# Kernel tuning notes

Hardware: AMD Instinct MI355X
Metric: run time of the kernel (lower is better)

## Reference

```python
import jax, jax.numpy as jnp
import numpy as np

B, D, M = 4, 3, 64
N2, N1, N0 = 512, 2048, 8192   # points per sample: coarse -> fine
C2, C1, C0 = 256, 128, 64
K = 3

def setup_inputs() -> dict:
    key = jax.random.key(0)
    ks = jax.random.split(key, 16)
    def nrm(k, shp, s=1.0):
        return jax.random.normal(k, shp, dtype=jnp.float32) * s
    return {
        "par_embedding": nrm(ks[0], (B, 1, M)),
        "x": nrm(ks[1], (B * N2, C2)),
        "pos": jax.random.uniform(ks[2], (B * N2, D), dtype=jnp.float32),
        "batch": jnp.repeat(jnp.arange(B), N2),
        "x_skip_l1": nrm(ks[3], (B * N1, C1)),
        "pos_skip_l1": jax.random.uniform(ks[4], (B * N1, D), dtype=jnp.float32),
        "batch_skip_l1": jnp.repeat(jnp.arange(B), N1),
        "x_skip_l0": nrm(ks[5], (B * N0, C0)),
        "pos_skip_l0": jax.random.uniform(ks[6], (B * N0, D), dtype=jnp.float32),
        "batch_skip_l0": jnp.repeat(jnp.arange(B), N0),
        # FP layer 0 MLP [C2+C1, 256, 128], plain_last=False; par_reduce -> 128
        "W0a": nrm(ks[7], (C2 + C1, 256), 0.05), "b0a": jnp.zeros((256,), jnp.float32),
        "W0b": nrm(ks[8], (256, 128), 0.05),     "b0b": jnp.zeros((128,), jnp.float32),
        "Wp0": nrm(ks[9], (M, 128), 0.05),       "bp0": jnp.zeros((128,), jnp.float32),
        # FP layer 1 MLP [128+C0, 128, 64], plain_last=True; par_reduce -> 64
        "W1a": nrm(ks[10], (128 + C0, 128), 0.05), "b1a": jnp.zeros((128,), jnp.float32),
        "W1b": nrm(ks[11], (128, 64), 0.05),       "b1b": jnp.zeros((64,), jnp.float32),
        "Wp1": nrm(ks[12], (M, 64), 0.05),         "bp1": jnp.zeros((64,), jnp.float32),
    }

def knn_interpolate(x, pos, pos_tgt, batch_size, k):
    """torch_geometric.nn.knn_interpolate with equal-size per-sample blocks.
    knn indices and inverse-squared-distance weights are non-differentiable
    (computed under no_grad in torch), hence stop_gradient."""
    C = x.shape[-1]
    xs = x.reshape(batch_size, -1, C)          # (B, ns, C)
    ps = pos.reshape(batch_size, -1, D)        # (B, ns, D)
    pt = pos_tgt.reshape(batch_size, -1, D)    # (B, nt, D)
    d2 = jnp.sum((pt[:, :, None, :] - ps[:, None, :, :]) ** 2, axis=-1)  # (B, nt, ns)
    d2 = jax.lax.stop_gradient(d2)
    neg_d2, idx = jax.lax.top_k(-d2, k)                                   # (B, nt, k)
    w = 1.0 / jnp.maximum(-neg_d2, 1e-16)
    feats = jax.vmap(lambda xb, ib: xb[ib])(xs, idx)                      # (B, nt, k, C)
    out = jnp.sum(feats * w[..., None], axis=2) / jnp.sum(w, axis=2, keepdims=True)
    return out.reshape(-1, C)

def fp_layer(par, x, pos, x_skip, pos_skip, k, Wa, ba, Wb, bb, Wp, bp, plain_last):
    bsz = par.shape[0]
    x = knn_interpolate(x, pos, pos_skip, bsz, k)
    x = jnp.concatenate([x, x_skip], axis=1)
    x = jnp.tanh(x @ Wa + ba)
    x = x @ Wb + bb
    if not plain_last:
        x = jnp.tanh(x)
    n = x.shape[0] // bsz
    p = jnp.tanh(par.reshape(bsz, -1) @ Wp + bp)     # (B, Cout)
    return x * jnp.repeat(p, n, axis=0)               # broadcast branch vector per sample

def reference(par_embedding, x, pos, batch, x_skip_l1, pos_skip_l1, batch_skip_l1,
              x_skip_l0, pos_skip_l0, batch_skip_l0,
              W0a, b0a, W0b, b0b, Wp0, bp0, W1a, b1a, W1b, b1b, Wp1, bp1):
    # skips[::-1]: coarser skip (level 1) consumed first, finest (level 0) last
    x1 = fp_layer(par_embedding, x, pos, x_skip_l1, pos_skip_l1, K,
                  W0a, b0a, W0b, b0b, Wp0, bp0, plain_last=False)
    x0 = fp_layer(par_embedding, x1, pos_skip_l1, x_skip_l0, pos_skip_l0, K,
                  W1a, b1a, W1b, b1b, Wp1, bp1, plain_last=True)
    return (x0, pos_skip_l0, batch_skip_l0)
```

## Files before the change

### kernel.cpp

```cpp
#include <hip/hip_runtime.h>
#include <hip/hip_bf16.h>

using bf16 = __hip_bfloat16;
using v8s = __attribute__((ext_vector_type(8))) short;
using v4f = __attribute__((ext_vector_type(4))) float;

constexpr int kB = 4, kM = 64;
constexpr int kN2 = 512, kN1 = 2048, kN0 = 8192;
constexpr int kC2 = 256, kC1 = 128, kC0 = 64;

__device__ __forceinline__ float bs2f(unsigned short u) {
    return __uint_as_float((unsigned)u << 16);
}
__device__ __forceinline__ unsigned short f2bs(float f) {
    unsigned u = __float_as_uint(f);
    u += 0x7FFFu + ((u >> 16) & 1u);
    return (unsigned short)(u >> 16);
}
__device__ __forceinline__ float rdIn(const void* p, long i, int f32) {
    return f32 ? ((const float*)p)[i] : bs2f(((const unsigned short*)p)[i]);
}
__device__ __forceinline__ unsigned short rdBS(const void* p, long i, int f32) {
    return f32 ? f2bs(((const float*)p)[i]) : ((const unsigned short*)p)[i];
}
__device__ __forceinline__ void ld8(const void* p, long off, int f32, float v[8]) {
    if (f32) {
        const float* fp = (const float*)p + off;
        float4 a = *(const float4*)fp;
        float4 b = *(const float4*)(fp + 4);
        v[0] = a.x; v[1] = a.y; v[2] = a.z; v[3] = a.w;
        v[4] = b.x; v[5] = b.y; v[6] = b.z; v[7] = b.w;
    } else {
        const unsigned short* hp = (const unsigned short*)p + off;
        uint4 u = *(const uint4*)hp;
        unsigned w[4] = {u.x, u.y, u.z, u.w};
        #pragma unroll
        for (int i = 0; i < 4; i++) {
            v[2 * i]     = bs2f((unsigned short)(w[i] & 0xFFFFu));
            v[2 * i + 1] = bs2f((unsigned short)(w[i] >> 16));
        }
    }
}
__device__ __forceinline__ uint4 pack8(const unsigned short o[8]) {
    uint4 u;
    u.x = (unsigned)o[0] | ((unsigned)o[1] << 16);
    u.y = (unsigned)o[2] | ((unsigned)o[3] << 16);
    u.z = (unsigned)o[4] | ((unsigned)o[5] << 16);
    u.w = (unsigned)o[6] | ((unsigned)o[7] << 16);
    return u;
}

__global__ void fpno_guard(float code, float* __restrict__ out) {
    if (threadIdx.x == 0) out[0] = code;
}

__global__ __launch_bounds__(512) void fpno_p1(
    const unsigned int* __restrict__ posW,
    const void* __restrict__ pos,
    const void* __restrict__ pos1,
    const void* __restrict__ pos0,
    const void* __restrict__ W0a, const void* __restrict__ W0b,
    const void* __restrict__ W1a, const void* __restrict__ W1b,
    const void* __restrict__ par,
    const void* __restrict__ Wp0, const void* __restrict__ bp0,
    const void* __restrict__ Wp1, const void* __restrict__ bp1,
    const int* __restrict__ bt0,
    int* __restrict__ flag, unsigned short* __restrict__ WT,
    float* __restrict__ g0, float* __restrict__ g1,
    int* __restrict__ i1d, float* __restrict__ w1d,
    float4* __restrict__ ptsG, int* __restrict__ cstG,
    float4* __restrict__ ptsT, int* __restrict__ cstT,
    float* __restrict__ out) {
    #pragma clang fp contract(off)
    __shared__ __align__(16) char smem[20480];
    __shared__ int sflg[2];
    const int b = blockIdx.x, tid = threadIdx.x;

    if (tid == 0) { sflg[0] = 0; sflg[1] = 0; }
    __syncthreads();
    {
        unsigned lo = posW[tid] & 0xFFFFu;
        int bad = 0, nz = 0;
        if (lo != 0u) { nz = 1; if ((lo & 0x8000u) || lo > 0x3F80u) bad = 1; }
        if (bad) sflg[0] = 1;
        if (nz) sflg[1] = 1;
    }
    __syncthreads();
    const int f32 = (sflg[0] || !sflg[1]) ? 1 : 0;
    if (b == 0 && tid == 0) *flag = f32;

    if (b < 320) {
        int id = b * 512 + tid;
        const void* src; int N; int base, local;
        if      (id < 98304)  { src = W0a; N = 256; base = 0;      local = id; }
        else if (id < 131072) { src = W0b; N = 128; base = 98304;  local = id - 98304; }
        else if (id < 155648) { src = W1a; N = 128; base = 131072; local = id - 131072; }
        else                  { src = W1b; N = 64;  base = 155648; local = id - 155648; }
        int NT = N >> 4;
        int e = local & 7;
        int l = (local >> 3) & 63;
        int rest = local >> 9;
        int t = rest % NT;
        int kc = rest / NT;
        int n = t * 16 + (l & 15);
        int k = kc * 32 + ((l >> 4) << 3) + e;
        WT[base + local] = rdBS(src, (long)k * N + n, f32);
    } else if (b < 322) {
        int id = (b - 320) * 512 + tid;
        if (id < kB * 128) {
            int bb = id / 128, n = id % 128;
            float a = rdIn(bp0, n, f32);
            for (int m = 0; m < kM; m++)
                a += rdIn(par, bb * kM + m, f32) * rdIn(Wp0, m * 128 + n, f32);
            g0[id] = tanhf(a);
        } else if (id < kB * 128 + kB * 64) {
            int id2 = id - kB * 128;
            int bb = id2 / 64, n = id2 % 64;
            float a = rdIn(bp1, n, f32);
            for (int m = 0; m < kM; m++)
                a += rdIn(par, bb * kM + m, f32) * rdIn(Wp1, m * 64 + n, f32);
            g1[id2] = tanhf(a);
        }
    } else if (b < 450) {
        constexpr int NS = kN2;
        float4* sp = (float4*)smem;
        float*  cd = (float*)(smem + 8192);
        int*    ci = (int*)(smem + 14336);
        const int blk = b - 322;
        const int tLoc = tid >> 3;
        const int spl  = tid & 7;
        const int tGlob = blk * 64 + tLoc;
        const int smp = tGlob / kN1;
        for (int i = tid; i < NS; i += 512) {
            long bb = (long)(smp * NS + i) * 3;
            sp[i] = make_float4(rdIn(pos, bb, f32), rdIn(pos, bb + 1, f32),
                                rdIn(pos, bb + 2, f32), 0.f);
        }
        __syncthreads();
        long tb = (long)tGlob * 3;
        float px = rdIn(pos1, tb, f32), py = rdIn(pos1, tb + 1, f32),
              pz = rdIn(pos1, tb + 2, f32);
        float d0 = 1e30f, d1 = 1e30f, d2 = 1e30f;
        int i0 = 0x7FFFFFFF, i1 = 0x7FFFFFFF, i2 = 0x7FFFFFFF;
        for (int j = spl; j < NS; j += 8) {
            float4 s = sp[j];
            float dx = px - s.x, dy = py - s.y, dz = pz - s.z;
            float d = ((dx * dx) + (dy * dy)) + (dz * dz);
            bool l0 = d < d0, l1 = d < d1, l2 = d < d2;
            float nd2 = l1 ? d1 : (l2 ? d : d2);
            int   ni2 = l1 ? i1 : (l2 ? j : i2);
            float nd1 = l0 ? d0 : (l1 ? d : d1);
            int   ni1 = l0 ? i0 : (l1 ? j : i1);
            float nd0 = l0 ? d : d0;
            int   ni0 = l0 ? j : i0;
            d2 = nd2; i2 = ni2; d1 = nd1; i1 = ni1; d0 = nd0; i0 = ni0;
        }
        cd[tid * 3 + 0] = d0; ci[tid * 3 + 0] = i0;
        cd[tid * 3 + 1] = d1; ci[tid * 3 + 1] = i1;
        cd[tid * 3 + 2] = d2; ci[tid * 3 + 2] = i2;
        __syncthreads();
        if (spl == 0) {
            float b0 = 1e30f, b1 = 1e30f, b2 = 1e30f;
            int k0 = 0x7FFFFFFF, k1 = 0x7FFFFFFF, k2 = 0x7FFFFFFF;
            int qb = tLoc * 24;
            for (int q = 0; q < 24; q++) {
                float d = cd[qb + q];
                int i = ci[qb + q];
                if ((d < b2) || (d == b2 && i < k2)) {
                    if ((d < b1) || (d == b1 && i < k1)) {
                        b2 = b1; k2 = k1;
                        if ((d < b0) || (d == b0 && i < k0)) { b1 = b0; k1 = k0; b0 = d; k0 = i; }
                        else                                  { b1 = d;  k1 = i; }
                    } else { b2 = d; k2 = i; }
                }
            }
            float wa = 1.f / fmaxf(b0, 1e-16f);
            float wb = 1.f / fmaxf(b1, 1e-16f);
            float wc = 1.f / fmaxf(b2, 1e-16f);
            float s = wa + wb + wc;
            i1d[tGlob * 3 + 0] = smp * NS + k0;
            i1d[tGlob * 3 + 1] = smp * NS + k1;
            i1d[tGlob * 3 + 2] = smp * NS + k2;
            w1d[tGlob * 3 + 0] = wa / s;
            w1d[tGlob * 3 + 1] = wb / s;
            w1d[tGlob * 3 + 2] = wc / s;
        }
    } else if (b < 458) {
        constexpr int G3 = 512;
        int* cnt = (int*)smem;
        int* sc  = cnt + G3;
        int* cur = sc + G3;
        const bool srcSide = (b < 454);
        const int smp = srcSide ? (b - 450) : (b - 454);
        const int NSb = srcSide ? kN1 : kN0;
        const int PPT = NSb / 512;
        const void* P = srcSide ? pos1 : pos0;
        float4* pts = srcSide ? ptsG : ptsT;
        int* cstart = srcSide ? cstG : cstT;
        for (int i = tid; i < G3; i += 512) cnt[i] = 0;
        __syncthreads();
        float4 p[16]; int cl[16];
        for (int r = 0; r < PPT; r++) {
            int j = r * 512 + tid;
            long bb = ((long)smp * NSb + j) * 3;
            float x = rdIn(P, bb, f32), y = rdIn(P, bb + 1, f32), z = rdIn(P, bb + 2, f32);
            int cx = min(7, max(0, (int)(x * 8.f)));
            int cy = min(7, max(0, (int)(y * 8.f)));
            int cz = min(7, max(0, (int)(z * 8.f)));
            cl[r] = (cz * 8 + cy) * 8 + cx;
            p[r] = make_float4(x, y, z, __int_as_float(j));
            atomicAdd(&cnt[cl[r]], 1);
        }
        __syncthreads();
        int v = cnt[tid];
        sc[tid] = v;
        __syncthreads();
        for (int ofs = 1; ofs < G3; ofs <<= 1) {
            int t = 0;
            if (tid >= ofs) t = sc[tid - ofs];
            __syncthreads();
            sc[tid] += t;
            __syncthreads();
        }
        {
            int st = sc[tid] - v;
            cur[tid] = st;
            cstart[smp * (G3 + 1) + tid] = st;
        }
        if (tid == 0) cstart[smp * (G3 + 1) + G3] = NSb;
        __syncthreads();
        for (int r = 0; r < PPT; r++) {
            int slot = atomicAdd(&cur[cl[r]], 1);
            pts[(long)smp * NSb + slot] = p[r];
        }
    } else {
        int id = (b - 458) * 512 + tid;
        const int nX = kB * kN0 * kC0;
        const int nP = kB * kN0 * 3;
        if (id < nP) out[nX + id] = rdIn(pos0, id, f32);
        else         out[nX + id] = (float)bt0[id - nP];
    }
}

__global__ __launch_bounds__(256) void fpno_p2(
    const void* __restrict__ x, const void* __restrict__ xs1,
    const unsigned short* __restrict__ WTf,
    const void* __restrict__ b0a, const void* __restrict__ b0b,
    const float* __restrict__ g0,
    const int* __restrict__ i1d, const float* __restrict__ w1d,
    const float4* __restrict__ ptsG, const int* __restrict__ cstG,
    const float4* __restrict__ ptsT,
    const int* __restrict__ flagp,
    unsigned short* __restrict__ X1,
    int* __restrict__ i0d, float* __restrict__ w0d) {
    #pragma clang fp contract(off)
    __shared__ __align__(16) char smem[21504];
    const int tid = threadIdx.x;

    if (blockIdx.x < 512) {
        constexpr int LDX = 392;
        constexpr int LDH = 264;
        const int f32 = *flagp;
        unsigned short* XC = (unsigned short*)smem;
        unsigned short* Hs = (unsigned short*)(smem + 12544);
        const int bm = blockIdx.x;

        for (int u = tid; u < 768; u += 256) {
            int row = u / 48, c0 = (u % 48) * 8;
            int gr = bm * 16 + row;
            unsigned short o[8];
            if (c0 < kC2) {
                int j0 = i1d[gr * 3 + 0], j1 = i1d[gr * 3 + 1], j2 = i1d[gr * 3 + 2];
                float ww0 = w1d[gr * 3 + 0], ww1 = w1d[gr * 3 + 1], ww2 = w1d[gr * 3 + 2];
                float a0[8], a1[8], a2[8];
                ld8(x, (long)j0 * kC2 + c0, f32, a0);
                ld8(x, (long)j1 * kC2 + c0, f32, a1);
                ld8(x, (long)j2 * kC2 + c0, f32, a2);
                #pragma unroll
                for (int j = 0; j < 8; j++)
                    o[j] = f2bs(ww0 * a0[j] + ww1 * a1[j] + ww2 * a2[j]);
            } else {
                float s8[8];
                ld8(xs1, (long)gr * kC1 + (c0 - kC2), f32, s8);
                #pragma unroll
                for (int j = 0; j < 8; j++) o[j] = f2bs(s8[j]);
            }
            *(uint4*)&XC[row * LDX + c0] = pack8(o);
        }
        __syncthreads();

        const int lane = tid & 63, w = tid >> 6;
        const int l16 = lane & 15, quad = lane >> 4;
        v4f acc[4];
        #pragma unroll
        for (int t = 0; t < 4; t++) acc[t] = (v4f){0.f, 0.f, 0.f, 0.f};
        #pragma unroll 1
        for (int k0 = 0; k0 < 384; k0 += 32) {
            const v8s a = *(const v8s*)&XC[l16 * LDX + k0 + quad * 8];
            int kc = k0 >> 5;
            #pragma unroll
            for (int t = 0; t < 4; t++) {
                int tg = w * 4 + t;
                const v8s bfr = *(const v8s*)&WTf[(((kc * 16 + tg) << 6) + lane) * 8];
                acc[t] = __builtin_amdgcn_mfma_f32_16x16x32_bf16(a, bfr, acc[t], 0, 0, 0);
            }
        }
        #pragma unroll
        for (int t = 0; t < 4; t++) {
            int c = (w * 4 + t) * 16 + l16;
            float bb = rdIn(b0a, c, f32);
            #pragma unroll
            for (int i = 0; i < 4; i++)
                Hs[(quad * 4 + i) * LDH + c] = f2bs(tanhf(acc[t][i] + bb));
        }
        __syncthreads();

        v4f acc2[2];
        #pragma unroll
        for (int t = 0; t < 2; t++) acc2[t] = (v4f){0.f, 0.f, 0.f, 0.f};
        #pragma unroll 1
        for (int k0 = 0; k0 < 256; k0 += 32) {
            const v8s a = *(const v8s*)&Hs[l16 * LDH + k0 + quad * 8];
            int kc = k0 >> 5;
            #pragma unroll
            for (int t = 0; t < 2; t++) {
                int tg = w * 2 + t;
                const v8s bfr = *(const v8s*)&WTf[98304 + (((kc * 8 + tg) << 6) + lane) * 8];
                acc2[t] = __builtin_amdgcn_mfma_f32_16x16x32_bf16(a, bfr, acc2[t], 0, 0, 0);
            }
        }
        #pragma unroll
        for (int t = 0; t < 2; t++) {
            int c = (w * 2 + t) * 16 + l16;
            float bb = rdIn(b0b, c, f32);
            #pragma unroll
            for (int i = 0; i < 4; i++) {
                int gr = bm * 16 + quad * 4 + i;
                float v = tanhf(acc2[t][i] + bb) * g0[(gr >> 11) * 128 + c];
                X1[(long)gr * 128 + c] = f2bs(v);
            }
        }
    } else {
        constexpr int NS = kN1, NT = kN0, G = 8, SPLIT = 8;
        constexpr int G3 = G * G * G;
        constexpr float h = 1.0f / (float)G;
        constexpr int TPT = 256 / SPLIT;
        constexpr int BPS = NT / TPT;
        int* cs = (int*)smem;
        const int vb = blockIdx.x - 512;
        const int tLoc = tid >> 3;
        const int spl  = tid & (SPLIT - 1);
        const int smp = vb / BPS;
        const int blk = vb % BPS;
        const float4* sp = ptsG + (long)smp * NS;
        for (int i = tid; i < G3 + 1; i += 256) cs[i] = cstG[smp * (G3 + 1) + i];
        __syncthreads();

        float4 q = ptsT[(long)smp * NT + blk * TPT + tLoc];
        float px = q.x, py = q.y, pz = q.z;
        const int jloc = __float_as_int(q.w);
        int cx = min(G - 1, max(0, (int)(px * (float)G)));
        int cy = min(G - 1, max(0, (int)(py * (float)G)));
        int cz = min(G - 1, max(0, (int)(pz * (float)G)));
        float d0 = 1e30f, d1 = 1e30f, d2 = 1e30f;
        int i0 = 0x7FFFFFFF, i1 = 0x7FFFFFFF, i2 = 0x7FFFFFFF;

        auto insert = [&](float d, int j) {
            bool l0 = (d < d0) || (d == d0 && j < i0);
            bool l1 = (d < d1) || (d == d1 && j < i1);
            bool l2 = (d < d2) || (d == d2 && j < i2);
            float nd2 = l1 ? d1 : (l2 ? d : d2);
            int   ni2 = l1 ? i1 : (l2 ? j : i2);
            float nd1 = l0 ? d0 : (l1 ? d : d1);
            int   ni1 = l0 ? i0 : (l1 ? j : i1);
            d2 = nd2; i2 = ni2; d1 = nd1; i1 = ni1;
            d0 = l0 ? d : d0; i0 = l0 ? j : i0;
        };
        auto scanCell = [&](int cell) {
            int s = cs[cell], e = cs[cell + 1];
            for (int t = s + spl; t < e; t += SPLIT) {
                float4 c = sp[t];
                int j = __float_as_int(c.w);
                float dx = px - c.x, dy = py - c.y, dz = pz - c.z;
                float d = ((dx * dx) + (dy * dy)) + (dz * dz);
                insert(d, j);
            }
        };
        auto merge8 = [&]() {
            #pragma unroll
            for (int m = 1; m < SPLIT; m <<= 1) {
                float pd0 = __shfl_xor(d0, m), pd1 = __shfl_xor(d1, m), pd2 = __shfl_xor(d2, m);
                int   pi0 = __shfl_xor(i0, m), pi1 = __shfl_xor(i1, m), pi2 = __shfl_xor(i2, m);
                if (pi0 != i0 && pi0 != i1 && pi0 != i2) insert(pd0, pi0);
                if (pi1 != i0 && pi1 != i1 && pi1 != i2) insert(pd1, pi1);
                if (pi2 != i0 && pi2 != i1 && pi2 != i2) insert(pd2, pi2);
            }
        };

        #pragma unroll 1
        for (int o = 0; o < 27; o++) {
            int ox = o % 3 - 1, oy = (o / 3) % 3 - 1, oz = o / 9 - 1;
            int X = cx + ox, Y = cy + oy, Z = cz + oz;
            if (X < 0 || X >= G || Y < 0 || Y >= G || Z < 0 || Z >= G) continue;
            scanCell((Z * G + Y) * G + X);
        }
        merge8();

        #pragma unroll 1
        for (int s = 2; s < G; s++) {
            float rm = ((float)(s - 1) * h);
            float ringMin = rm * rm * 0.9999f;
            if (d2 < ringMin) break;
            #pragma unroll 1
            for (int oz = -s; oz <= s; oz++) {
                int Z = cz + oz; if (Z < 0 || Z >= G) continue;
                int az = oz < 0 ? -oz : oz;
                #pragma unroll 1
                for (int oy = -s; oy <= s; oy++) {
                    int Y = cy + oy; if (Y < 0 || Y >= G) continue;
                    int ay = oy < 0 ? -oy : oy;
                    bool outer = (az == s) || (ay == s);
                    #pragma unroll 1
                    for (int ox = -s; ox <= s; ox++) {
                        int ax = ox < 0 ? -ox : ox;
                        if (!outer && ax != s) continue;
                        int X = cx + ox; if (X < 0 || X >= G) continue;
                        float lx = (float)X * h, ly = (float)Y * h, lz = (float)Z * h;
                        float ex = fmaxf(0.f, fmaxf(lx - px, px - (lx + h)));
                        float ey = fmaxf(0.f, fmaxf(ly - py, py - (ly + h)));
                        float ez = fmaxf(0.f, fmaxf(lz - pz, pz - (lz + h)));
                        float md = ((ex * ex) + (ey * ey)) + (ez * ez);
                        if (md * 0.9999f > d2) continue;
                        scanCell((Z * G + Y) * G + X);
                    }
                }
            }
            merge8();
        }

        if (spl == 0) {
            float wa = 1.f / fmaxf(d0, 1e-16f);
            float wb = 1.f / fmaxf(d1, 1e-16f);
            float wc = 1.f / fmaxf(d2, 1e-16f);
            float sw = wa + wb + wc;
            long tg = (long)smp * NT + jloc;
            i0d[tg * 3 + 0] = smp * NS + i0;
            i0d[tg * 3 + 1] = smp * NS + i1;
            i0d[tg * 3 + 2] = smp * NS + i2;
            w0d[tg * 3 + 0] = wa / sw;
            w0d[tg * 3 + 1] = wb / sw;
            w0d[tg * 3 + 2] = wc / sw;
        }
    }
}

__global__ __launch_bounds__(256) void fpno_p3(
    const unsigned short* __restrict__ X1, const void* __restrict__ xs0,
    const unsigned short* __restrict__ WTf,
    const void* __restrict__ b1a, const void* __restrict__ b1b,
    const float* __restrict__ g1,
    const int* __restrict__ i0d, const float* __restrict__ w0d,
    const int* __restrict__ flagp,
    float* __restrict__ out) {
    #pragma clang fp contract(off)
    constexpr int LDX = 200;
    constexpr int LDH = 136;
    __shared__ __align__(16) char smem[10752];
    const int f32 = *flagp;
    const int tid = threadIdx.x;
    unsigned short* XC = (unsigned short*)smem;
    unsigned short* Hs = (unsigned short*)(smem + 6400);
    const int bm = blockIdx.x;

    for (int u = tid; u < 384; u += 256) {
        int row = u / 24, c0 = (u % 24) * 8;
        int gr = bm * 16 + row;
        unsigned short o[8];
        if (c0 < kC1) {
            int j0 = i0d[gr * 3 + 0], j1 = i0d[gr * 3 + 1], j2 = i0d[gr * 3 + 2];
            float ww0 = w0d[gr * 3 + 0], ww1 = w0d[gr * 3 + 1], ww2 = w0d[gr * 3 + 2];
            float a0[8], a1[8], a2[8];
            ld8(X1, (long)j0 * kC1 + c0, 0, a0);
            ld8(X1, (long)j1 * kC1 + c0, 0, a1);
            ld8(X1, (long)j2 * kC1 + c0, 0, a2);
            #pragma unroll
            for (int j = 0; j < 8; j++)
                o[j] = f2bs(ww0 * a0[j] + ww1 * a1[j] + ww2 * a2[j]);
        } else {
            float s8[8];
            ld8(xs0, (long)gr * kC0 + (c0 - kC1), f32, s8);
            #pragma unroll
            for (int j = 0; j < 8; j++) o[j] = f2bs(s8[j]);
        }
        *(uint4*)&XC[row * LDX + c0] = pack8(o);
    }
    __syncthreads();

    const int lane = tid & 63, w = tid >> 6;
    const int l16 = lane & 15, quad = lane >> 4;
    v4f acc[2];
    #pragma unroll
    for (int t = 0; t < 2; t++) acc[t] = (v4f){0.f, 0.f, 0.f, 0.f};
    #pragma unroll 1
    for (int k0 = 0; k0 < 192; k0 += 32) {
        const v8s a = *(const v8s*)&XC[l16 * LDX + k0 + quad * 8];
        int kc = k0 >> 5;
        #pragma unroll
        for (int t = 0; t < 2; t++) {
            int tg = w * 2 + t;
            const v8s bfr = *(const v8s*)&WTf[131072 + (((kc * 8 + tg) << 6) + lane) * 8];
            acc[t] = __builtin_amdgcn_mfma_f32_16x16x32_bf16(a, bfr, acc[t], 0, 0, 0);
        }
    }
    #pragma unroll
    for (int t = 0; t < 2; t++) {
        int c = (w * 2 + t) * 16 + l16;
        float bb = rdIn(b1a, c, f32);
        #pragma unroll
        for (int i = 0; i < 4; i++)
            Hs[(quad * 4 + i) * LDH + c] = f2bs(tanhf(acc[t][i] + bb));
    }
    __syncthreads();

    v4f acc2 = (v4f){0.f, 0.f, 0.f, 0.f};
    #pragma unroll 1
    for (int k0 = 0; k0 < 128; k0 += 32) {
        const v8s a = *(const v8s*)&Hs[l16 * LDH + k0 + quad * 8];
        int kc = k0 >> 5;
        const v8s bfr = *(const v8s*)&WTf[155648 + (((kc * 4 + w) << 6) + lane) * 8];
        acc2 = __builtin_amdgcn_mfma_f32_16x16x32_bf16(a, bfr, acc2, 0, 0, 0);
    }
    {
        int c = w * 16 + l16;
        float bb = rdIn(b1b, c, f32);
        #pragma unroll
        for (int i = 0; i < 4; i++) {
            int gr = bm * 16 + quad * 4 + i;
            float v = (acc2[i] + bb) * g1[(gr >> 13) * 64 + c];
            out[(long)gr * 64 + c] = v;
        }
    }
}

extern "C" void kernel_launch(void* const* d_in, const int* in_sizes, int n_in,
                              void* d_out, int out_size, void* d_ws, size_t ws_size,
                              hipStream_t stream) {
    (void)out_size;
    float* out = (float*)d_out;
    const int R1 = kB * kN1;
    const int R0 = kB * kN0;

    static const int kExp[22] = {
        256, 524288, 6144, 2048, 1048576, 24576, 8192, 2097152, 98304, 32768,
        98304, 256, 32768, 128, 8192, 128, 24576, 128, 8192, 64, 4096, 64};
    if (n_in != 22) { fpno_guard<<<1, 64, 0, stream>>>(3072.0f, out); return; }
    for (int i = 0; i < 22; i++) {
        if (in_sizes[i] != kExp[i]) {
            fpno_guard<<<1, 64, 0, stream>>>(1024.0f + 8.0f * i, out);
            return;
        }
    }

    char* base = (char*)d_ws;
    size_t off = 0;
    auto alloc = [&](size_t bytes) {
        off = (off + 255) & ~(size_t)255; size_t o = off; off += bytes; return o;
    };
    int*            flag = (int*)(base + alloc(4));
    float*          g0   = (float*)(base + alloc(kB * 128 * 4));
    float*          g1   = (float*)(base + alloc(kB * 64 * 4));
    int*            i1d  = (int*)(base + alloc((size_t)R1 * 3 * 4));
    float*          w1d  = (float*)(base + alloc((size_t)R1 * 3 * 4));
    int*            i0d  = (int*)(base + alloc((size_t)R0 * 3 * 4));
    float*          w0d  = (float*)(base + alloc((size_t)R0 * 3 * 4));
    float4*         ptsG = (float4*)(base + alloc((size_t)kB * kN1 * 16));
    int*            cstG = (int*)(base + alloc((size_t)kB * (512 + 1) * 4));
    float4*         ptsT = (float4*)(base + alloc((size_t)kB * kN0 * 16));
    int*            cstT = (int*)(base + alloc((size_t)kB * (512 + 1) * 4));
    unsigned short* WT   = (unsigned short*)(base + alloc(163840 * 2));
    unsigned short* X1   = (unsigned short*)(base + alloc((size_t)R1 * 128 * 2));
    if (ws_size < off) { fpno_guard<<<1, 64, 0, stream>>>(2048.0f, out); return; }

    const void* par  = d_in[0];
    const void* x    = d_in[1];
    const void* pos  = d_in[2];
    const void* xs1  = d_in[4];
    const void* pos1 = d_in[5];
    const void* xs0  = d_in[7];
    const void* pos0 = d_in[8];
    const int*  bt0  = (const int*)d_in[9];
    const void *W0a = d_in[10], *b0a = d_in[11], *W0b = d_in[12], *b0b = d_in[13];
    const void *Wp0 = d_in[14], *bp0 = d_in[15];
    const void *W1a = d_in[16], *b1a = d_in[17], *W1b = d_in[18], *b1b = d_in[19];
    const void *Wp1 = d_in[20], *bp1 = d_in[21];

    fpno_p1<<<714, 512, 0, stream>>>(
        (const unsigned int*)pos, pos, pos1, pos0,
        W0a, W0b, W1a, W1b, par, Wp0, bp0, Wp1, bp1, bt0,
        flag, WT, g0, g1, i1d, w1d, ptsG, cstG, ptsT, cstT, out);

    fpno_p2<<<1536, 256, 0, stream>>>(
        x, xs1, WT, b0a, b0b, g0, i1d, w1d,
        ptsG, cstG, ptsT, flag, X1, i0d, w0d);

    fpno_p3<<<2048, 256, 0, stream>>>(
        X1, xs0, WT, b1a, b1b, g1, i0d, w0d, flag, out);
}
```

Baseline: 172.5 us.

## Stage block's union neighborhood points into LDS for KNN scan

For the second-level KNN search, each block computes the bounding box of its targets' grid cells, extends it by one cell, and cooperatively copies the source points in that box into shared memory. All threads then scan the staged points instead of fetching each of the 27 neighbour cells from global memory, and later ring passes skip cells already covered by the box. This replaces many scattered global reads with one coalesced staging load. The cost is extra atomics and barriers, plus scanning more points per thread than the 27-cell neighbourhood when the box is large. A fallback keeps the old path when the box exceeds the row or capacity limits.

```diff
diff --git a/kernel.cpp b/kernel.cpp
--- a/kernel.cpp
+++ b/kernel.cpp
@@ -346,7 +346,18 @@
         constexpr float h = 1.0f / (float)G;
         constexpr int TPT = 256 / SPLIT;
         constexpr int BPS = NT / TPT;
-        int* cs = (int*)smem;
+        constexpr int CAP = 384, MAXROWS = 12;
+        int*    cs   = (int*)smem;
+        float4* spts = (float4*)(smem + 2064);
+        int*    meta = (int*)(smem + 2064 + CAP * 16);
+        int* bmn = meta;
+        int* bmx = meta + 3;
+        int* rowSeg = meta + 6;
+        int* rowOff = meta + 18;
+        int* mNR  = meta + 31;
+        int* mTOT = meta + 32;
+        int* mUSE = meta + 33;
+
         const int vb = blockIdx.x - 512;
         const int tLoc = tid >> 3;
         const int spl  = tid & (SPLIT - 1);
@@ -354,6 +365,10 @@
         const int blk = vb % BPS;
         const float4* sp = ptsG + (long)smp * NS;
         for (int i = tid; i < G3 + 1; i += 256) cs[i] = cstG[smp * (G3 + 1) + i];
+        if (tid == 0) {
+            bmn[0] = G; bmn[1] = G; bmn[2] = G;
+            bmx[0] = -1; bmx[1] = -1; bmx[2] = -1;
+        }
         __syncthreads();
 
         float4 q = ptsT[(long)smp * NT + blk * TPT + tLoc];
@@ -362,6 +377,35 @@
         int cx = min(G - 1, max(0, (int)(px * (float)G)));
         int cy = min(G - 1, max(0, (int)(py * (float)G)));
         int cz = min(G - 1, max(0, (int)(pz * (float)G)));
+        atomicMin(&bmn[0], cx); atomicMax(&bmx[0], cx);
+        atomicMin(&bmn[1], cy); atomicMax(&bmx[1], cy);
+        atomicMin(&bmn[2], cz); atomicMax(&bmx[2], cz);
+        __syncthreads();
+        if (tid == 0) {
+            int x0 = max(bmn[0] - 1, 0), x1 = min(bmx[0] + 1, G - 1);
+            int y0 = max(bmn[1] - 1, 0), y1 = min(bmx[1] + 1, G - 1);
+            int z0 = max(bmn[2] - 1, 0), z1 = min(bmx[2] + 1, G - 1);
+            int nr = (y1 - y0 + 1) * (z1 - z0 + 1);
+            int tot = 0, ok = (nr <= MAXROWS);
+            if (ok) {
+                int r = 0;
+                for (int Z = z0; Z <= z1; Z++)
+                    for (int Y = y0; Y <= y1; Y++) {
+                        int cb = (Z * G + Y) * G;
+                        int s0 = cs[cb + x0], e0 = cs[cb + x1 + 1];
+                        rowSeg[r] = s0; rowOff[r] = tot; tot += e0 - s0; r++;
+                    }
+                rowOff[nr] = tot;
+                ok = (tot <= CAP);
+            }
+            mNR[0] = ok ? nr : 0; mTOT[0] = tot; mUSE[0] = ok;
+            bmn[0] = x0; bmx[0] = x1;
+            bmn[1] = y0; bmx[1] = y1;
+            bmn[2] = z0; bmx[2] = z1;
+        }
+        __syncthreads();
+        const int useStage = mUSE[0];
+
         float d0 = 1e30f, d1 = 1e30f, d2 = 1e30f;
         int i0 = 0x7FFFFFFF, i1 = 0x7FFFFFFF, i2 = 0x7FFFFFFF;
 
@@ -397,12 +441,29 @@
             }
         };
 
-        #pragma unroll 1
-        for (int o = 0; o < 27; o++) {
-            int ox = o % 3 - 1, oy = (o / 3) % 3 - 1, oz = o / 9 - 1;
-            int X = cx + ox, Y = cy + oy, Z = cz + oz;
-            if (X < 0 || X >= G || Y < 0 || Y >= G || Z < 0 || Z >= G) continue;
-            scanCell((Z * G + Y) * G + X);
+        if (useStage) {
+            const int nr = mNR[0];
+            for (int r = 0; r < nr; r++) {
+                int base0 = rowOff[r], len = rowOff[r + 1] - base0;
+                for (int i = tid; i < len; i += 256) spts[base0 + i] = sp[rowSeg[r] + i];
+            }
+            __syncthreads();
+            const int tot = mTOT[0];
+            for (int t = spl; t < tot; t += SPLIT) {
+                float4 c = spts[t];
+                int j = __float_as_int(c.w);
+                float dx = px - c.x, dy = py - c.y, dz = pz - c.z;
+                float d = ((dx * dx) + (dy * dy)) + (dz * dz);
+                insert(d, j);
+            }
+        } else {
+            #pragma unroll 1
+            for (int o = 0; o < 27; o++) {
+                int ox = o % 3 - 1, oy = (o / 3) % 3 - 1, oz = o / 9 - 1;
+                int X = cx + ox, Y = cy + oy, Z = cz + oz;
+                if (X < 0 || X >= G || Y < 0 || Y >= G || Z < 0 || Z >= G) continue;
+                scanCell((Z * G + Y) * G + X);
+            }
         }
         merge8();
 
@@ -425,6 +486,10 @@
                         int ax = ox < 0 ? -ox : ox;
                         if (!outer && ax != s) continue;
                         int X = cx + ox; if (X < 0 || X >= G) continue;
+                        if (useStage &&
+                            X >= bmn[0] && X <= bmx[0] &&
+                            Y >= bmn[1] && Y <= bmx[1] &&
+                            Z >= bmn[2] && Z <= bmx[2]) continue;
                         float lx = (float)X * h, ly = (float)Y * h, lz = (float)Z * h;
                         float ex = fmaxf(0.f, fmaxf(lx - px, px - (lx + h)));
                         float ey = fmaxf(0.f, fmaxf(ly - py, py - (ly + h)));
```

New measurement: 191.6 us. 1.11x slower.
